# Kernel tuning notes

Measured on AMD Instinct MI355X. Metric: run time of the kernel, lower is better.

## Reference

```python
import jax, jax.numpy as jnp
import numpy as np

B, T, F_SEQ, F_TAB = 512, 1024, 64, 128
H_SEQ, H_TAB = 128, 128


def setup_inputs() -> dict:
    key = jax.random.key(0)
    ks = jax.random.split(key, 10)
    s = lambda fan_in: 1.0 / np.sqrt(fan_in)
    return {
        "tabular_data": jax.random.normal(ks[0], (B, F_TAB), jnp.float32),
        "sequence_data": jax.random.normal(ks[1], (B, T, F_SEQ), jnp.float32),
        # LSTM params, PyTorch gate order (i, f, g, o)
        "W_ih": jax.random.uniform(ks[2], (4 * H_SEQ, F_SEQ), jnp.float32, -s(H_SEQ), s(H_SEQ)),
        "W_hh": jax.random.uniform(ks[3], (4 * H_SEQ, H_SEQ), jnp.float32, -s(H_SEQ), s(H_SEQ)),
        "b_ih": jax.random.uniform(ks[4], (4 * H_SEQ,), jnp.float32, -s(H_SEQ), s(H_SEQ)),
        "b_hh": jax.random.uniform(ks[5], (4 * H_SEQ,), jnp.float32, -s(H_SEQ), s(H_SEQ)),
        # tabular branch
        "W_tab": jax.random.uniform(ks[6], (H_TAB, F_TAB), jnp.float32, -s(F_TAB), s(F_TAB)),
        "b_tab": jax.random.uniform(ks[7], (H_TAB,), jnp.float32, -s(F_TAB), s(F_TAB)),
        # output head
        "W_out": jax.random.uniform(ks[8], (2, H_SEQ + H_TAB), jnp.float32, -s(H_SEQ + H_TAB), s(H_SEQ + H_TAB)),
        "b_out": jax.random.uniform(ks[9], (2,), jnp.float32, -s(H_SEQ + H_TAB), s(H_SEQ + H_TAB)),
    }


def _lstm_last(seq, W_ih, W_hh, b_ih, b_hh):
    # seq: [B, T, F]; returns last hidden state [B, H]
    Bn = seq.shape[0]
    H = W_hh.shape[1]
    # precompute input projections for all timesteps: [T, B, 4H]
    x_proj = jnp.einsum('btf,gf->tbg', seq, W_ih) + (b_ih + b_hh)

    def step(carry, xp):
        h, c = carry
        gates = xp + h @ W_hh.T  # [B, 4H]
        i, f, g, o = jnp.split(gates, 4, axis=-1)
        i = jax.nn.sigmoid(i)
        f = jax.nn.sigmoid(f)
        g = jnp.tanh(g)
        o = jax.nn.sigmoid(o)
        c = f * c + i * g
        h = o * jnp.tanh(c)
        return (h, c), None

    init = (jnp.zeros((Bn, H), seq.dtype), jnp.zeros((Bn, H), seq.dtype))
    (h, _), _ = jax.lax.scan(step, init, x_proj)
    return h


def reference(tabular_data, sequence_data, W_ih, W_hh, b_ih, b_hh, W_tab, b_tab, W_out, b_out):
    lstm_last = _lstm_last(sequence_data, W_ih, W_hh, b_ih, b_hh)  # [B, H_SEQ]
    tab = jax.nn.relu(tabular_data @ W_tab.T + b_tab)  # [B, H_TAB]
    combined = jnp.concatenate([lstm_last, tab], axis=1)
    logits = combined @ W_out.T + b_out  # [B, 2]
    return logits
```

## Files before the change

### kernel.cpp

```cpp
#include <hip/hip_runtime.h>
#include <hip/hip_bf16.h>


typedef __attribute__((ext_vector_type(8))) short bf16x8;
typedef __attribute__((ext_vector_type(4))) float f32x4;

#define LOG2E 1.44269504088896340736f

__device__ __forceinline__ float fexp2(float x) {
#if __has_builtin(__builtin_amdgcn_exp2f)
    return __builtin_amdgcn_exp2f(x);
#else
    float r; asm("v_exp_f32 %0, %1" : "=v"(r) : "v"(x)); return r;
#endif
}
__device__ __forceinline__ float frcp(float x) {
#if __has_builtin(__builtin_amdgcn_rcpf)
    return __builtin_amdgcn_rcpf(x);
#else
    float r; asm("v_rcp_f32 %0, %1" : "=v"(r) : "v"(x)); return r;
#endif
}
__device__ __forceinline__ float sigm2(float xs) { return frcp(1.0f + fexp2(-xs)); }

__device__ __forceinline__ short bf16b(float x) {
    __hip_bfloat16 h = __float2bfloat16(x);
    short r; __builtin_memcpy(&r, &h, 2); return r;
}

__global__ __launch_bounds__(512, 2)
void lstm_fused(const float* __restrict__ tabular,
                const float* __restrict__ seq,
                const float* __restrict__ W_ih,
                const float* __restrict__ W_hh,
                const float* __restrict__ b_ih,
                const float* __restrict__ b_hh,
                const float* __restrict__ W_tab,
                const float* __restrict__ b_tab,
                const float* __restrict__ W_out,
                const float* __restrict__ b_out,
                float* __restrict__ out)
{
    constexpr int HSTRIDE = 136;
    constexpr int SSTRIDE = 72;
    __shared__ short hbuf[2][16 * HSTRIDE];
    __shared__ short sbuf[2][8 * 16 * SSTRIDE];
    __shared__ float hff[16][132];
    __shared__ float tbf[16][132];

    const int tid  = threadIdx.x;
    const int lane = tid & 63;
    const int wid  = tid >> 6;
    const int l15  = lane & 15;
    const int q    = lane >> 4;
    const int b0   = blockIdx.x * 16;
    const int u    = wid * 16 + l15;

    bf16x8 whh[4][4];
    bf16x8 wih[4][2];
    float  bias[4];
#pragma unroll
    for (int nt = 0; nt < 4; ++nt) {
        const int g = nt * 128 + u;
        const float s = (nt == 2) ? (2.0f * LOG2E) : LOG2E;
        bias[nt] = (b_ih[g] + b_hh[g]) * s;
#pragma unroll
        for (int kc = 0; kc < 4; ++kc) {
            const float* p = W_hh + g * 128 + kc * 32 + q * 8;
            bf16x8 fr;
#pragma unroll
            for (int j = 0; j < 8; ++j) fr[j] = bf16b(p[j] * s);
            whh[nt][kc] = fr;
        }
#pragma unroll
        for (int kc = 0; kc < 2; ++kc) {
            const float* p = W_ih + g * 64 + kc * 32 + q * 8;
            bf16x8 fr;
#pragma unroll
            for (int j = 0; j < 8; ++j) fr[j] = bf16b(p[j] * s);
            wih[nt][kc] = fr;
        }
    }

    for (int i = tid; i < 16 * HSTRIDE; i += 512) hbuf[1][i] = 0;

    const int sr  = tid >> 5;
    const int sub = tid & 31;
    const int stt = sub >> 2;
    const int sk0 = (sub & 3) * 16;

    {
        const float* p = seq + ((size_t)(b0 + sr) * 1024 + stt) * 64 + sk0;
        f32x4 ld[4];
#pragma unroll
        for (int i = 0; i < 4; ++i) ld[i] = ((const f32x4*)p)[i];
        short* dst = &sbuf[0][(stt * 16 + sr) * SSTRIDE + sk0];
        bf16x8 a, b;
#pragma unroll
        for (int i = 0; i < 8; ++i) a[i] = bf16b(ld[i >> 2][i & 3]);
#pragma unroll
        for (int i = 0; i < 8; ++i) b[i] = bf16b(ld[2 + (i >> 2)][i & 3]);
        *(bf16x8*)dst       = a;
        *(bf16x8*)(dst + 8) = b;
    }
    __syncthreads();

    float cc[4] = {0.f, 0.f, 0.f, 0.f};
    float hl[4] = {0.f, 0.f, 0.f, 0.f};

    f32x4 xacc[4];
    {
        const short* sb0 = sbuf[0];
        bf16x8 x0 = *(const bf16x8*)(sb0 + l15 * SSTRIDE + q * 8);
        bf16x8 x1 = *(const bf16x8*)(sb0 + l15 * SSTRIDE + 32 + q * 8);
#pragma unroll
        for (int nt = 0; nt < 4; ++nt) {
            f32x4 a = {bias[nt], bias[nt], bias[nt], bias[nt]};
            a = __builtin_amdgcn_mfma_f32_16x16x32_bf16(x0, wih[nt][0], a, 0, 0, 0);
            a = __builtin_amdgcn_mfma_f32_16x16x32_bf16(x1, wih[nt][1], a, 0, 0, 0);
            xacc[nt] = a;
        }
    }

#pragma unroll 1
    for (int ch = 0; ch < 128; ++ch) {
        f32x4 pend[4];
#pragma unroll
        for (int tt = 0; tt < 8; ++tt) {
            if (tt == 0 && ch + 1 < 128) {
                const float* p = seq + ((size_t)(b0 + sr) * 1024 + (size_t)(ch + 1) * 8 + stt) * 64 + sk0;
#pragma unroll
                for (int i = 0; i < 4; ++i) pend[i] = ((const f32x4*)p)[i];
            }

            const short* hb = hbuf[(tt + 1) & 1];
            bf16x8 hA[4];
#pragma unroll
            for (int kc = 0; kc < 4; ++kc)
                hA[kc] = *(const bf16x8*)(hb + l15 * HSTRIDE + kc * 32 + q * 8);

            f32x4 gt[4];
#pragma unroll
            for (int nt = 0; nt < 4; ++nt) {
                f32x4 a = xacc[nt];
#pragma unroll
                for (int kc = 0; kc < 4; ++kc)
                    a = __builtin_amdgcn_mfma_f32_16x16x32_bf16(hA[kc], whh[nt][kc], a, 0, 0, 0);
                gt[nt] = a;
            }

            if (tt < 7 || ch < 127) {
                const int tn   = ch * 8 + tt + 1;
                const short* sbn = sbuf[(tn >> 3) & 1];
                const int rowb = ((tn & 7) * 16 + l15) * SSTRIDE;
                bf16x8 x0 = *(const bf16x8*)(sbn + rowb + q * 8);
                bf16x8 x1 = *(const bf16x8*)(sbn + rowb + 32 + q * 8);
#pragma unroll
                for (int nt = 0; nt < 4; ++nt) {
                    f32x4 a = {bias[nt], bias[nt], bias[nt], bias[nt]};
                    a = __builtin_amdgcn_mfma_f32_16x16x32_bf16(x0, wih[nt][0], a, 0, 0, 0);
                    a = __builtin_amdgcn_mfma_f32_16x16x32_bf16(x1, wih[nt][1], a, 0, 0, 0);
                    xacc[nt] = a;
                }
            }

            if (tt == 4 && ch + 1 < 128) {
                short* dst = &sbuf[(ch + 1) & 1][(stt * 16 + sr) * SSTRIDE + sk0];
                bf16x8 a, b;
#pragma unroll
                for (int i = 0; i < 8; ++i) a[i] = bf16b(pend[i >> 2][i & 3]);
#pragma unroll
                for (int i = 0; i < 8; ++i) b[i] = bf16b(pend[2 + (i >> 2)][i & 3]);
                *(bf16x8*)dst       = a;
                *(bf16x8*)(dst + 8) = b;
            }

            short* hw = hbuf[tt & 1];
#pragma unroll
            for (int j = 0; j < 4; ++j) {
                float ig = sigm2(gt[0][j]);
                float fg = sigm2(gt[1][j]);
                float gg = 2.0f * sigm2(gt[2][j]) - 1.0f;
                float og = sigm2(gt[3][j]);
                float c  = fg * cc[j] + ig * gg;
                cc[j] = c;
                float th = 2.0f * sigm2(c * (2.0f * LOG2E)) - 1.0f;
                float h  = og * th;
                hl[j] = h;
                hw[(4 * q + j) * HSTRIDE + u] = bf16b(h);
            }
            __syncthreads();
        }
    }

#pragma unroll
    for (int j = 0; j < 4; ++j) hff[4 * q + j][u] = hl[j];
    __syncthreads();

    {
        const int r   = tid >> 5;
        const int un0 = (tid & 31) * 4;
        const float* trow = tabular + (size_t)(b0 + r) * 128;
        float a0 = b_tab[un0], a1 = b_tab[un0 + 1], a2 = b_tab[un0 + 2], a3 = b_tab[un0 + 3];
        const float* w0 = W_tab + (un0 + 0) * 128;
        const float* w1 = W_tab + (un0 + 1) * 128;
        const float* w2 = W_tab + (un0 + 2) * 128;
        const float* w3 = W_tab + (un0 + 3) * 128;
#pragma unroll 4
        for (int f = 0; f < 128; f += 4) {
            f32x4 tv = *(const f32x4*)(trow + f);
            f32x4 v0 = *(const f32x4*)(w0 + f);
            f32x4 v1 = *(const f32x4*)(w1 + f);
            f32x4 v2 = *(const f32x4*)(w2 + f);
            f32x4 v3 = *(const f32x4*)(w3 + f);
#pragma unroll
            for (int e = 0; e < 4; ++e) {
                a0 += tv[e] * v0[e];
                a1 += tv[e] * v1[e];
                a2 += tv[e] * v2[e];
                a3 += tv[e] * v3[e];
            }
        }
        tbf[r][un0]     = fmaxf(a0, 0.f);
        tbf[r][un0 + 1] = fmaxf(a1, 0.f);
        tbf[r][un0 + 2] = fmaxf(a2, 0.f);
        tbf[r][un0 + 3] = fmaxf(a3, 0.f);
    }
    __syncthreads();

    if (tid < 32) {
        const int r = tid >> 1, o = tid & 1;
        const float* w = W_out + o * 256;
        float a = b_out[o];
#pragma unroll 8
        for (int j = 0; j < 128; ++j) a += hff[r][j] * w[j];
#pragma unroll 8
        for (int j = 0; j < 128; ++j) a += tbf[r][j] * w[128 + j];
        out[(size_t)(b0 + r) * 2 + o] = a;
    }
}

extern "C" void kernel_launch(void* const* d_in, const int* in_sizes, int n_in,
                              void* d_out, int out_size, void* d_ws, size_t ws_size,
                              hipStream_t stream) {
    const float* tabular = (const float*)d_in[0];
    const float* seq     = (const float*)d_in[1];
    const float* W_ih    = (const float*)d_in[2];
    const float* W_hh    = (const float*)d_in[3];
    const float* b_ih    = (const float*)d_in[4];
    const float* b_hh    = (const float*)d_in[5];
    const float* W_tab   = (const float*)d_in[6];
    const float* b_tab   = (const float*)d_in[7];
    const float* W_out   = (const float*)d_in[8];
    const float* b_out   = (const float*)d_in[9];
    float* o = (float*)d_out;
    hipLaunchKernelGGL(lstm_fused, dim3(32), dim3(512), 0, stream,
                       tabular, seq, W_ih, W_hh, b_ih, b_hh, W_tab, b_tab, W_out, b_out, o);
}
```

Before: 1.008 ms.

## Swizzle LDS layouts, fuse gate reciprocals, packed bf16 stores, lighter barrier

Drops the padded strides on the h and sequence LDS buffers in favour of XOR-swizzled unpadded layouts, with all read and write offsets precomputed once. The gate math folds the sign into the scaled weights and merges reciprocal pairs: input·tanh(g) and output·tanh(c) each use a single rcp. bf16 conversion now goes through packed pair conversions. The barrier becomes an LDS-only waitcnt plus s_barrier, and the MFMA section runs at raised wave priority. The aim is to shorten the serial per-timestep critical path, with some risk of swizzle indexing mistakes and of overflow in the merged reciprocal products.

```diff
diff --git a/kernel.cpp b/kernel.cpp
--- a/kernel.cpp
+++ b/kernel.cpp
@@ -4,8 +4,10 @@
 
 typedef __attribute__((ext_vector_type(8))) short bf16x8;
 typedef __attribute__((ext_vector_type(4))) float f32x4;
+typedef __attribute__((ext_vector_type(4))) unsigned int u32x4;
 
 #define LOG2E 1.44269504088896340736f
+#define NEG2L (-2.0f * LOG2E)
 
 __device__ __forceinline__ float fexp2(float x) {
 #if __has_builtin(__builtin_amdgcn_exp2f)
@@ -21,11 +23,26 @@
     float r; asm("v_rcp_f32 %0, %1" : "=v"(r) : "v"(x)); return r;
 #endif
 }
-__device__ __forceinline__ float sigm2(float xs) { return frcp(1.0f + fexp2(-xs)); }
-
+
+__device__ __forceinline__ unsigned int pk_bf16(float a, float b) {
+    float2 f2; f2.x = a; f2.y = b;
+    __hip_bfloat162 h = __float22bfloat162_rn(f2);
+    unsigned int r; __builtin_memcpy(&r, &h, 4); return r;
+}
 __device__ __forceinline__ short bf16b(float x) {
     __hip_bfloat16 h = __float2bfloat16(x);
     short r; __builtin_memcpy(&r, &h, 2); return r;
+}
+
+__device__ __forceinline__ void st8(short* dst, const f32x4 a, const f32x4 b) {
+    u32x4 v = { pk_bf16(a[0], a[1]), pk_bf16(a[2], a[3]),
+                pk_bf16(b[0], b[1]), pk_bf16(b[2], b[3]) };
+    *(u32x4*)dst = v;
+}
+
+__device__ __forceinline__ void block_sync_lds() {
+    asm volatile("s_waitcnt lgkmcnt(0)" ::: "memory");
+    __builtin_amdgcn_s_barrier();
 }
 
 __global__ __launch_bounds__(512, 2)
@@ -41,10 +58,8 @@
                 const float* __restrict__ b_out,
                 float* __restrict__ out)
 {
-    constexpr int HSTRIDE = 136;
-    constexpr int SSTRIDE = 72;
-    __shared__ short hbuf[2][16 * HSTRIDE];
-    __shared__ short sbuf[2][8 * 16 * SSTRIDE];
+    __shared__ short hbuf[2][16 * 128];
+    __shared__ short sbuf[2][8 * 16 * 64];
     __shared__ float hff[16][132];
     __shared__ float tbf[16][132];
 
@@ -62,7 +77,7 @@
 #pragma unroll
     for (int nt = 0; nt < 4; ++nt) {
         const int g = nt * 128 + u;
-        const float s = (nt == 2) ? (2.0f * LOG2E) : LOG2E;
+        const float s = (nt == 2) ? (-2.0f * LOG2E) : (-LOG2E);
         bias[nt] = (b_ih[g] + b_hh[g]) * s;
 #pragma unroll
         for (int kc = 0; kc < 4; ++kc) {
@@ -82,26 +97,38 @@
         }
     }
 
-    for (int i = tid; i < 16 * HSTRIDE; i += 512) hbuf[1][i] = 0;
+    int hroff[4];
+#pragma unroll
+    for (int kc = 0; kc < 4; ++kc)
+        hroff[kc] = l15 * 128 + (((kc * 4 + q) ^ (l15 & 7)) << 3);
+    int hwoff[4];
+#pragma unroll
+    for (int j = 0; j < 4; ++j) {
+        const int r = 4 * q + j;
+        hwoff[j] = r * 128 + ((((u >> 3) ^ (r & 7))) << 3) + (u & 7);
+    }
+    int xroff[2];
+#pragma unroll
+    for (int kc = 0; kc < 2; ++kc)
+        xroff[kc] = l15 * 64 + (((kc * 4 + q) ^ (l15 & 7)) << 3);
 
     const int sr  = tid >> 5;
     const int sub = tid & 31;
     const int stt = sub >> 2;
-    const int sk0 = (sub & 3) * 16;
+    const int k4  = sub & 3;
+    const float* sbase = seq + ((size_t)(b0 + sr) * 1024 + stt) * 64 + k4 * 16;
+    const int srow = stt * 16 + sr;
+    const int ws0 = srow * 64 + (((2 * k4)     ^ (sr & 7)) << 3);
+    const int ws1 = srow * 64 + (((2 * k4 + 1) ^ (sr & 7)) << 3);
+
+    for (int i = tid; i < 16 * 128; i += 512) hbuf[1][i] = 0;
 
     {
-        const float* p = seq + ((size_t)(b0 + sr) * 1024 + stt) * 64 + sk0;
         f32x4 ld[4];
 #pragma unroll
-        for (int i = 0; i < 4; ++i) ld[i] = ((const f32x4*)p)[i];
-        short* dst = &sbuf[0][(stt * 16 + sr) * SSTRIDE + sk0];
-        bf16x8 a, b;
-#pragma unroll
-        for (int i = 0; i < 8; ++i) a[i] = bf16b(ld[i >> 2][i & 3]);
-#pragma unroll
-        for (int i = 0; i < 8; ++i) b[i] = bf16b(ld[2 + (i >> 2)][i & 3]);
-        *(bf16x8*)dst       = a;
-        *(bf16x8*)(dst + 8) = b;
+        for (int i = 0; i < 4; ++i) ld[i] = ((const f32x4*)sbase)[i];
+        st8(&sbuf[0][ws0], ld[0], ld[1]);
+        st8(&sbuf[0][ws1], ld[2], ld[3]);
     }
     __syncthreads();
 
@@ -111,8 +138,8 @@
     f32x4 xacc[4];
     {
         const short* sb0 = sbuf[0];
-        bf16x8 x0 = *(const bf16x8*)(sb0 + l15 * SSTRIDE + q * 8);
-        bf16x8 x1 = *(const bf16x8*)(sb0 + l15 * SSTRIDE + 32 + q * 8);
+        bf16x8 x0 = *(const bf16x8*)(sb0 + xroff[0]);
+        bf16x8 x1 = *(const bf16x8*)(sb0 + xroff[1]);
 #pragma unroll
         for (int nt = 0; nt < 4; ++nt) {
             f32x4 a = {bias[nt], bias[nt], bias[nt], bias[nt]};
@@ -128,7 +155,7 @@
 #pragma unroll
         for (int tt = 0; tt < 8; ++tt) {
             if (tt == 0 && ch + 1 < 128) {
-                const float* p = seq + ((size_t)(b0 + sr) * 1024 + (size_t)(ch + 1) * 8 + stt) * 64 + sk0;
+                const float* p = sbase + (size_t)(ch + 1) * 512;
 #pragma unroll
                 for (int i = 0; i < 4; ++i) pend[i] = ((const f32x4*)p)[i];
             }
@@ -137,8 +164,9 @@
             bf16x8 hA[4];
 #pragma unroll
             for (int kc = 0; kc < 4; ++kc)
-                hA[kc] = *(const bf16x8*)(hb + l15 * HSTRIDE + kc * 32 + q * 8);
-
+                hA[kc] = *(const bf16x8*)(hb + hroff[kc]);
+
+            __builtin_amdgcn_s_setprio(1);
             f32x4 gt[4];
 #pragma unroll
             for (int nt = 0; nt < 4; ++nt) {
@@ -152,9 +180,9 @@
             if (tt < 7 || ch < 127) {
                 const int tn   = ch * 8 + tt + 1;
                 const short* sbn = sbuf[(tn >> 3) & 1];
-                const int rowb = ((tn & 7) * 16 + l15) * SSTRIDE;
-                bf16x8 x0 = *(const bf16x8*)(sbn + rowb + q * 8);
-                bf16x8 x1 = *(const bf16x8*)(sbn + rowb + 32 + q * 8);
+                const int tb   = (tn & 7) * 1024;
+                bf16x8 x0 = *(const bf16x8*)(sbn + tb + xroff[0]);
+                bf16x8 x1 = *(const bf16x8*)(sbn + tb + xroff[1]);
 #pragma unroll
                 for (int nt = 0; nt < 4; ++nt) {
                     f32x4 a = {bias[nt], bias[nt], bias[nt], bias[nt]};
@@ -163,33 +191,37 @@
                     xacc[nt] = a;
                 }
             }
+            __builtin_amdgcn_s_setprio(0);
 
             if (tt == 4 && ch + 1 < 128) {
-                short* dst = &sbuf[(ch + 1) & 1][(stt * 16 + sr) * SSTRIDE + sk0];
-                bf16x8 a, b;
-#pragma unroll
-                for (int i = 0; i < 8; ++i) a[i] = bf16b(pend[i >> 2][i & 3]);
-#pragma unroll
-                for (int i = 0; i < 8; ++i) b[i] = bf16b(pend[2 + (i >> 2)][i & 3]);
-                *(bf16x8*)dst       = a;
-                *(bf16x8*)(dst + 8) = b;
+                short* d = sbuf[(ch + 1) & 1];
+                st8(d + ws0, pend[0], pend[1]);
+                st8(d + ws1, pend[2], pend[3]);
             }
 
             short* hw = hbuf[tt & 1];
 #pragma unroll
             for (int j = 0; j < 4; ++j) {
-                float ig = sigm2(gt[0][j]);
-                float fg = sigm2(gt[1][j]);
-                float gg = 2.0f * sigm2(gt[2][j]) - 1.0f;
-                float og = sigm2(gt[3][j]);
-                float c  = fg * cc[j] + ig * gg;
+                float ei = fexp2(gt[0][j]);
+                float ef = fexp2(gt[1][j]);
+                float eg = fexp2(gt[2][j]);
+                float eo = fexp2(gt[3][j]);
+                float fg   = frcp(1.0f + ef);
+                float igg  = (1.0f - eg) * frcp((1.0f + eg) * (1.0f + ei));
+                float c    = __builtin_fmaf(fg, cc[j], igg);
                 cc[j] = c;
-                float th = 2.0f * sigm2(c * (2.0f * LOG2E)) - 1.0f;
-                float h  = og * th;
-                hl[j] = h;
-                hw[(4 * q + j) * HSTRIDE + u] = bf16b(h);
-            }
-            __syncthreads();
+                float ec = fexp2(c * NEG2L);
+                hl[j] = (1.0f - ec) * frcp((1.0f + ec) * (1.0f + eo));
+            }
+            {
+                unsigned int p01 = pk_bf16(hl[0], hl[1]);
+                unsigned int p23 = pk_bf16(hl[2], hl[3]);
+                hw[hwoff[0]] = (short)p01;
+                hw[hwoff[1]] = (short)(p01 >> 16);
+                hw[hwoff[2]] = (short)p23;
+                hw[hwoff[3]] = (short)(p23 >> 16);
+            }
+            block_sync_lds();
         }
     }
 
```

Result: no change. 995.1 us (-1.2%).
